# Optimization experiments

Measured on AMD Instinct MI355X. Metric: run time of the kernel, lower is better.

## Reference

```python
import jax, jax.numpy as jnp
import numpy as np

N, E = 50000, 800000
F_IN, HID, NCLS = 128, 128, 64
EPS = 1e-6


def setup_inputs() -> dict:
    key = jax.random.key(0)
    ks = jax.random.split(key, 6)
    x = jax.random.normal(ks[0], (N, F_IN), dtype=jnp.float32)
    edge_index = jax.random.randint(ks[1], (2, E), 0, N, dtype=jnp.int32)
    # GCNConv glorot init
    W1 = jax.random.normal(ks[2], (F_IN, HID), dtype=jnp.float32) * np.sqrt(2.0 / (F_IN + HID))
    b1 = jnp.zeros((HID,), jnp.float32)
    gamma1 = jnp.ones((HID,), jnp.float32)
    beta1 = jnp.zeros((HID,), jnp.float32)
    W2 = jax.random.normal(ks[3], (HID, NCLS), dtype=jnp.float32) * np.sqrt(2.0 / (HID + NCLS))
    b2 = jnp.zeros((NCLS,), jnp.float32)
    return {"x": x, "edge_index": edge_index, "W1": W1, "b1": b1,
            "gamma1": gamma1, "beta1": beta1, "W2": W2, "b2": b2}


def _gcn_conv(x, src, dst, norm, W, b, n):
    # x' = A_hat @ (x W) + b, A_hat = D^-1/2 (A+I) D^-1/2
    h = x @ W                                   # [N, out]
    msg = h[src] * norm[:, None]                # [E+N, out] gather
    out = jax.ops.segment_sum(msg, dst, num_segments=n)  # scatter-add
    return out + b


def _layer_norm(h, gamma, beta):
    mu = jnp.mean(h, axis=-1, keepdims=True)
    var = jnp.mean(jnp.square(h - mu), axis=-1, keepdims=True)
    return (h - mu) * jax.lax.rsqrt(var + EPS) * gamma + beta


def reference(x, edge_index, W1, b1, gamma1, beta1, W2, b2):
    n = x.shape[0]
    loop = jnp.arange(n, dtype=edge_index.dtype)
    src = jnp.concatenate([edge_index[0], loop])  # add self loops
    dst = jnp.concatenate([edge_index[1], loop])
    deg = jax.ops.segment_sum(jnp.ones_like(dst, jnp.float32), dst, num_segments=n)
    dinv = jnp.where(deg > 0, jax.lax.rsqrt(deg), 0.0)
    norm = dinv[src] * dinv[dst]                 # [E+N]
    h = _gcn_conv(x, src, dst, norm, W1, b1, n)
    h = jax.nn.relu(_layer_norm(h, gamma1, beta1))
    out = _gcn_conv(h, src, dst, norm, W2, b2, n)
    return out
```

## Files before the change

### kernel.cpp

```cpp
#include <hip/hip_runtime.h>


typedef float f32x2 __attribute__((ext_vector_type(2)));
typedef float f32x4 __attribute__((ext_vector_type(4)));
typedef unsigned u32x4 __attribute__((ext_vector_type(4)));
typedef __bf16 bf16x8 __attribute__((ext_vector_type(8)));

__device__ __forceinline__ unsigned short f2bf(float f) {
    unsigned u = __float_as_uint(f);
    u += 0x7FFF + ((u >> 16) & 1);
    return (unsigned short)(u >> 16);
}
__device__ __forceinline__ float bfLo(unsigned g) { return __uint_as_float(g << 16); }
__device__ __forceinline__ float bfHi(unsigned g) { return __uint_as_float(g & 0xFFFF0000u); }

__global__ __launch_bounds__(256) void cvt_wi(const float* __restrict__ W1,
                                              const float* __restrict__ W2,
                                              unsigned short* __restrict__ W1t,
                                              unsigned short* __restrict__ W2t,
                                              int* __restrict__ cnt, int n) {
    int id = blockIdx.x * 256 + threadIdx.x;
    if (id < 128 * 128) {
        int c = id >> 7, k = id & 127;
        W1t[id] = f2bf(W1[k * 128 + c]);
    } else if (id < 128 * 128 + 64 * 128) {
        int j = id - 128 * 128;
        int c = j >> 7, k = j & 127;
        W2t[j] = f2bf(W2[k * 64 + c]);
    }
    if (id < n) cnt[id] = 0;
}

__global__ void count_k(const int* __restrict__ dst, int* __restrict__ cnt,
                        int* __restrict__ rank, int e) {
    int i = blockIdx.x * blockDim.x + threadIdx.x;
    if (i < e) {
        int r = atomicAdd(&cnt[dst[i]], 1);
        __builtin_nontemporal_store(r, &rank[i]);
    }
}

__global__ __launch_bounds__(1024) void scan1_k(const int* __restrict__ cnt,
                                                int* __restrict__ incl,
                                                int* __restrict__ bsum, int n) {
    __shared__ int lds[1024];
    int t = threadIdx.x;
    int i = blockIdx.x * 1024 + t;
    int v = (i < n) ? ((cnt[i] + 15) & ~15) : 0;
    lds[t] = v;
    __syncthreads();
#pragma unroll
    for (int d = 1; d < 1024; d <<= 1) {
        int u = (t >= d) ? lds[t - d] : 0;
        __syncthreads();
        lds[t] += u;
        __syncthreads();
    }
    if (i < n) incl[i] = lds[t];
    if (t == 1023) bsum[blockIdx.x] = lds[1023];
}

__global__ __launch_bounds__(1024) void scan3_k(const int* __restrict__ cnt,
                                                const int* __restrict__ incl,
                                                const int* __restrict__ bsum,
                                                int* __restrict__ offs,
                                                float* __restrict__ dinv,
                                                unsigned* __restrict__ epk,
                                                int nb, int n) {
    __shared__ int sP;
    int t = threadIdx.x, bid = blockIdx.x;
    if (t < 64) {
        int raw = (t < nb) ? bsum[t] : 0;
        int v = raw;
#pragma unroll
        for (int d = 1; d < 64; d <<= 1) {
            int u = __shfl_up(v, d);
            if (t >= d) v += u;
        }
        if (t == bid) sP = v - raw;
    }
    __syncthreads();
    int i = bid * 1024 + t;
    if (i >= n) return;
    int c = cnt[i];
    int c16 = (c + 15) & ~15;
    int inc = sP + incl[i];
    int ex = inc - c16;
    offs[i] = ex;
    dinv[i] = rsqrtf((float)(c + 1));
    for (int j = c; j < c16; ++j)
        __builtin_nontemporal_store(0u, &epk[ex + j]);
    if (i == n - 1) offs[n] = inc;
}

__device__ __forceinline__ void dev_fill(const int* __restrict__ src,
                                         const int* __restrict__ dst,
                                         const int* __restrict__ rank,
                                         const int* __restrict__ offs,
                                         const float* __restrict__ dinv,
                                         unsigned* __restrict__ epk, int e, int bid) {
    int i = bid * 256 + threadIdx.x;
    if (i >= e) return;
    int s = src[i], d = dst[i];
    float w = dinv[s] * dinv[d];
    epk[offs[d] + rank[i]] = ((unsigned)s << 16) | (unsigned)f2bf(w);
}

template<int NT, bool CVT>
__device__ __forceinline__ void dev_gemm(const void* __restrict__ Asrc,
                                         const uint4* __restrict__ Wt,
                                         unsigned short* __restrict__ tab,
                                         int n, int bid, uint4* As) {
    int t = threadIdx.x;
    int r0 = bid * 64;
    int rows = min(64, n - r0);
#pragma unroll
    for (int it = 0; it < 4; ++it) {
        int u = it * 256 + t;
        int row = u >> 4, s = u & 15;
        uint4 v = make_uint4(0u, 0u, 0u, 0u);
        if (row < rows) {
            if constexpr (CVT) {
                const float4* X4 = (const float4*)Asrc;
                float4 a = X4[(size_t)(r0 + row) * 32 + 2 * s];
                float4 b = X4[(size_t)(r0 + row) * 32 + 2 * s + 1];
                v.x = (unsigned)f2bf(a.x) | ((unsigned)f2bf(a.y) << 16);
                v.y = (unsigned)f2bf(a.z) | ((unsigned)f2bf(a.w) << 16);
                v.z = (unsigned)f2bf(b.x) | ((unsigned)f2bf(b.y) << 16);
                v.w = (unsigned)f2bf(b.z) | ((unsigned)f2bf(b.w) << 16);
            } else {
                v = ((const uint4*)Asrc)[(size_t)(r0 + row) * 16 + s];
            }
        }
        As[row * 16 + (s ^ (row & 7))] = v;
    }
    __syncthreads();

    int wv = t >> 6, lane = t & 63;
    int arow = lane & 15;
    int kg = lane >> 4;
    int lrow = wv * 16 + arow;

    f32x4 acc[NT];
    f32x4 z = {0.f, 0.f, 0.f, 0.f};
#pragma unroll
    for (int j = 0; j < NT; ++j) acc[j] = z;

#pragma unroll
    for (int ks = 0; ks < 4; ++ks) {
        bf16x8 a = __builtin_bit_cast(bf16x8,
                       As[lrow * 16 + ((ks * 4 + kg) ^ (arow & 7))]);
#pragma unroll
        for (int tl = 0; tl < NT; ++tl) {
            bf16x8 b = __builtin_bit_cast(bf16x8,
                           Wt[(size_t)(tl * 16 + arow) * 16 + ks * 4 + kg]);
            acc[tl] = __builtin_amdgcn_mfma_f32_16x16x32_bf16(a, b, acc[tl], 0, 0, 0);
        }
    }

    int grow0 = r0 + wv * 16 + 4 * kg;
#pragma unroll
    for (int r = 0; r < 4; ++r) {
        int grow = grow0 + r;
        if (grow < n) {
            unsigned short* rowp = tab + (size_t)grow * (NT * 16) + arow;
#pragma unroll
            for (int tl = 0; tl < NT; ++tl)
                rowp[tl * 16] = f2bf(acc[tl][r]);
        }
    }
}

__global__ __launch_bounds__(256) void fill_gemm1_k(const float* __restrict__ x,
                                                    const uint4* __restrict__ W1t,
                                                    unsigned short* __restrict__ h0b,
                                                    int n, int gb,
                                                    const int* __restrict__ src,
                                                    const int* __restrict__ dst,
                                                    const int* __restrict__ rank,
                                                    const int* __restrict__ offs,
                                                    const float* __restrict__ dinv,
                                                    unsigned* __restrict__ epk, int e) {
    __shared__ uint4 As[64 * 16];
    int bid = blockIdx.x;
    if (bid < gb)
        dev_gemm<8, true>(x, W1t, h0b, n, bid, As);
    else
        dev_fill(src, dst, rank, offs, dinv, epk, e, bid - gb);
}

__global__ __launch_bounds__(256) void gemm2_k(const unsigned* __restrict__ h1b,
                                               const uint4* __restrict__ W2t,
                                               unsigned short* __restrict__ tab,
                                               int n) {
    __shared__ uint4 As[64 * 16];
    dev_gemm<4, false>(h1b, W2t, tab, n, blockIdx.x, As);
}

__global__ __launch_bounds__(256) void prop_ln(const unsigned* __restrict__ h0b,
                                               const int* __restrict__ offs,
                                               const unsigned* __restrict__ epk,
                                               const float* __restrict__ dinv,
                                               const float* __restrict__ b1,
                                               const float* __restrict__ gamma,
                                               const float* __restrict__ beta,
                                               unsigned* __restrict__ h1b, int n) {
    int wid = __builtin_amdgcn_readfirstlane((blockIdx.x * blockDim.x + threadIdx.x) >> 6);
    int lane = threadIdx.x & 63;
    if (wid >= n) return;
    float di = dinv[wid];
    unsigned self = h0b[(size_t)wid * 64 + lane];
    float a0 = bfLo(self) * di * di;
    float a1 = bfHi(self) * di * di;

    int s0 = offs[wid], s1 = offs[wid + 1];
    if (s0 < s1) {
        const u32x4* ep4 = (const u32x4*)(epk + s0);
        int nb16 = (s1 - s0) >> 4;
        u32x4 d0 = __builtin_nontemporal_load(ep4);
        u32x4 d1 = __builtin_nontemporal_load(ep4 + 1);
        u32x4 d2 = __builtin_nontemporal_load(ep4 + 2);
        u32x4 d3 = __builtin_nontemporal_load(ep4 + 3);
        for (int b = 0; b < nb16; ++b) {
            unsigned g0  = h0b[(size_t)(d0.x >> 16) * 64 + lane];
            unsigned g1  = h0b[(size_t)(d0.y >> 16) * 64 + lane];
            unsigned g2  = h0b[(size_t)(d0.z >> 16) * 64 + lane];
            unsigned g3  = h0b[(size_t)(d0.w >> 16) * 64 + lane];
            unsigned g4  = h0b[(size_t)(d1.x >> 16) * 64 + lane];
            unsigned g5  = h0b[(size_t)(d1.y >> 16) * 64 + lane];
            unsigned g6  = h0b[(size_t)(d1.z >> 16) * 64 + lane];
            unsigned g7  = h0b[(size_t)(d1.w >> 16) * 64 + lane];
            unsigned g8  = h0b[(size_t)(d2.x >> 16) * 64 + lane];
            unsigned g9  = h0b[(size_t)(d2.y >> 16) * 64 + lane];
            unsigned g10 = h0b[(size_t)(d2.z >> 16) * 64 + lane];
            unsigned g11 = h0b[(size_t)(d2.w >> 16) * 64 + lane];
            unsigned g12 = h0b[(size_t)(d3.x >> 16) * 64 + lane];
            unsigned g13 = h0b[(size_t)(d3.y >> 16) * 64 + lane];
            unsigned g14 = h0b[(size_t)(d3.z >> 16) * 64 + lane];
            unsigned g15 = h0b[(size_t)(d3.w >> 16) * 64 + lane];
            float w0  = bfLo(d0.x), w1  = bfLo(d0.y), w2  = bfLo(d0.z), w3  = bfLo(d0.w);
            float w4  = bfLo(d1.x), w5  = bfLo(d1.y), w6  = bfLo(d1.z), w7  = bfLo(d1.w);
            float w8  = bfLo(d2.x), w9  = bfLo(d2.y), w10 = bfLo(d2.z), w11 = bfLo(d2.w);
            float w12 = bfLo(d3.x), w13 = bfLo(d3.y), w14 = bfLo(d3.z), w15 = bfLo(d3.w);
            int bn = (b + 1 < nb16) ? b + 1 : 0;
            d0 = __builtin_nontemporal_load(ep4 + 4 * bn);
            d1 = __builtin_nontemporal_load(ep4 + 4 * bn + 1);
            d2 = __builtin_nontemporal_load(ep4 + 4 * bn + 2);
            d3 = __builtin_nontemporal_load(ep4 + 4 * bn + 3);
            a0 = fmaf(bfLo(g0),  w0,  a0); a1 = fmaf(bfHi(g0),  w0,  a1);
            a0 = fmaf(bfLo(g1),  w1,  a0); a1 = fmaf(bfHi(g1),  w1,  a1);
            a0 = fmaf(bfLo(g2),  w2,  a0); a1 = fmaf(bfHi(g2),  w2,  a1);
            a0 = fmaf(bfLo(g3),  w3,  a0); a1 = fmaf(bfHi(g3),  w3,  a1);
            a0 = fmaf(bfLo(g4),  w4,  a0); a1 = fmaf(bfHi(g4),  w4,  a1);
            a0 = fmaf(bfLo(g5),  w5,  a0); a1 = fmaf(bfHi(g5),  w5,  a1);
            a0 = fmaf(bfLo(g6),  w6,  a0); a1 = fmaf(bfHi(g6),  w6,  a1);
            a0 = fmaf(bfLo(g7),  w7,  a0); a1 = fmaf(bfHi(g7),  w7,  a1);
            a0 = fmaf(bfLo(g8),  w8,  a0); a1 = fmaf(bfHi(g8),  w8,  a1);
            a0 = fmaf(bfLo(g9),  w9,  a0); a1 = fmaf(bfHi(g9),  w9,  a1);
            a0 = fmaf(bfLo(g10), w10, a0); a1 = fmaf(bfHi(g10), w10, a1);
            a0 = fmaf(bfLo(g11), w11, a0); a1 = fmaf(bfHi(g11), w11, a1);
            a0 = fmaf(bfLo(g12), w12, a0); a1 = fmaf(bfHi(g12), w12, a1);
            a0 = fmaf(bfLo(g13), w13, a0); a1 = fmaf(bfHi(g13), w13, a1);
            a0 = fmaf(bfLo(g14), w14, a0); a1 = fmaf(bfHi(g14), w14, a1);
            a0 = fmaf(bfLo(g15), w15, a0); a1 = fmaf(bfHi(g15), w15, a1);
        }
    }

    a0 += b1[2 * lane];
    a1 += b1[2 * lane + 1];
    float sum = a0 + a1, sq = a0 * a0 + a1 * a1;
#pragma unroll
    for (int off = 32; off > 0; off >>= 1) {
        sum += __shfl_xor(sum, off);
        sq  += __shfl_xor(sq, off);
    }
    float mu  = sum * (1.f / 128.f);
    float var = fmaxf(sq * (1.f / 128.f) - mu * mu, 0.f);
    float rstd = rsqrtf(var + 1e-6f);
    float y0 = fmaxf((a0 - mu) * rstd * gamma[2 * lane] + beta[2 * lane], 0.f);
    float y1 = fmaxf((a1 - mu) * rstd * gamma[2 * lane + 1] + beta[2 * lane + 1], 0.f);
    unsigned pk = (unsigned)f2bf(y0) | ((unsigned)f2bf(y1) << 16);
    __builtin_nontemporal_store(pk, &h1b[(size_t)wid * 64 + lane]);
}

__global__ __launch_bounds__(256) void prop_out(const unsigned* __restrict__ h2b,
                                                const int* __restrict__ offs,
                                                const unsigned* __restrict__ epk,
                                                const float* __restrict__ dinv,
                                                const float* __restrict__ b2,
                                                float* __restrict__ out, int n) {
    int wid = __builtin_amdgcn_readfirstlane((blockIdx.x * blockDim.x + threadIdx.x) >> 6);
    int lane = threadIdx.x & 63;
    if (wid >= n) return;
    int es = lane >> 5, u = lane & 31;
    float di = dinv[wid];
    float a0 = 0.f, a1 = 0.f;
    if (es == 0) {
        unsigned self = h2b[(size_t)wid * 32 + u];
        a0 = bfLo(self) * di * di;
        a1 = bfHi(self) * di * di;
    }

    int s0 = offs[wid], s1 = offs[wid + 1];
    if (s0 < s1) {
        const u32x4* ep4 = (const u32x4*)(epk + s0);
        int nb16 = (s1 - s0) >> 4;
        u32x4 d0 = __builtin_nontemporal_load(ep4);
        u32x4 d1 = __builtin_nontemporal_load(ep4 + 1);
        u32x4 d2 = __builtin_nontemporal_load(ep4 + 2);
        u32x4 d3 = __builtin_nontemporal_load(ep4 + 3);
        for (int b = 0; b < nb16; ++b) {
            unsigned dd0 = es ? d0.y : d0.x;
            unsigned dd1 = es ? d0.w : d0.z;
            unsigned dd2 = es ? d1.y : d1.x;
            unsigned dd3 = es ? d1.w : d1.z;
            unsigned dd4 = es ? d2.y : d2.x;
            unsigned dd5 = es ? d2.w : d2.z;
            unsigned dd6 = es ? d3.y : d3.x;
            unsigned dd7 = es ? d3.w : d3.z;
            unsigned g0 = h2b[(size_t)(dd0 >> 16) * 32 + u];
            unsigned g1 = h2b[(size_t)(dd1 >> 16) * 32 + u];
            unsigned g2 = h2b[(size_t)(dd2 >> 16) * 32 + u];
            unsigned g3 = h2b[(size_t)(dd3 >> 16) * 32 + u];
            unsigned g4 = h2b[(size_t)(dd4 >> 16) * 32 + u];
            unsigned g5 = h2b[(size_t)(dd5 >> 16) * 32 + u];
            unsigned g6 = h2b[(size_t)(dd6 >> 16) * 32 + u];
            unsigned g7 = h2b[(size_t)(dd7 >> 16) * 32 + u];
            float w0 = bfLo(dd0), w1 = bfLo(dd1), w2 = bfLo(dd2), w3 = bfLo(dd3);
            float w4 = bfLo(dd4), w5 = bfLo(dd5), w6 = bfLo(dd6), w7 = bfLo(dd7);
            int bn = (b + 1 < nb16) ? b + 1 : 0;
            d0 = __builtin_nontemporal_load(ep4 + 4 * bn);
            d1 = __builtin_nontemporal_load(ep4 + 4 * bn + 1);
            d2 = __builtin_nontemporal_load(ep4 + 4 * bn + 2);
            d3 = __builtin_nontemporal_load(ep4 + 4 * bn + 3);
            a0 = fmaf(bfLo(g0), w0, a0); a1 = fmaf(bfHi(g0), w0, a1);
            a0 = fmaf(bfLo(g1), w1, a0); a1 = fmaf(bfHi(g1), w1, a1);
            a0 = fmaf(bfLo(g2), w2, a0); a1 = fmaf(bfHi(g2), w2, a1);
            a0 = fmaf(bfLo(g3), w3, a0); a1 = fmaf(bfHi(g3), w3, a1);
            a0 = fmaf(bfLo(g4), w4, a0); a1 = fmaf(bfHi(g4), w4, a1);
            a0 = fmaf(bfLo(g5), w5, a0); a1 = fmaf(bfHi(g5), w5, a1);
            a0 = fmaf(bfLo(g6), w6, a0); a1 = fmaf(bfHi(g6), w6, a1);
            a0 = fmaf(bfLo(g7), w7, a0); a1 = fmaf(bfHi(g7), w7, a1);
        }
    }

    a0 += __shfl_xor(a0, 32);
    a1 += __shfl_xor(a1, 32);
    if (es == 0) {
        f32x2 o; o.x = a0 + b2[2 * u]; o.y = a1 + b2[2 * u + 1];
        __builtin_nontemporal_store(o, &((f32x2*)out)[(size_t)wid * 32 + u]);
    }
}

extern "C" void kernel_launch(void* const* d_in, const int* in_sizes, int n_in,
                              void* d_out, int out_size, void* d_ws, size_t ws_size,
                              hipStream_t stream) {
    const float* x     = (const float*)d_in[0];
    const int*   ei    = (const int*)d_in[1];
    const float* W1    = (const float*)d_in[2];
    const float* b1    = (const float*)d_in[3];
    const float* gam   = (const float*)d_in[4];
    const float* bet   = (const float*)d_in[5];
    const float* W2    = (const float*)d_in[6];
    const float* b2    = (const float*)d_in[7];
    float* out = (float*)d_out;

    int n = in_sizes[0] / 128;
    int e = in_sizes[1] / 2;
    const int* src = ei;
    const int* dst = ei + e;
    size_t ecap = (size_t)e + 16 * (size_t)n;

    char* p = (char*)d_ws;
    auto alloc = [&](size_t bytes) {
        void* q = (void*)p;
        p += (bytes + 255) & ~(size_t)255;
        return q;
    };
    int*            cnt  = (int*)alloc((size_t)n * 4);
    int*            offs = (int*)alloc((size_t)(n + 1) * 4);
    int*            rank = (int*)alloc((size_t)e * 4);
    float*          dinv = (float*)alloc((size_t)n * 4);
    int*            incl = (int*)alloc((size_t)n * 4);
    int*            bsum = (int*)alloc(64 * 4);
    unsigned*       epk  = (unsigned*)alloc(ecap * 4);
    unsigned*       h0b  = (unsigned*)alloc((size_t)n * 64 * 4);
    unsigned*       h1b  = (unsigned*)alloc((size_t)n * 64 * 4);
    unsigned short* W1t  = (unsigned short*)alloc(128 * 128 * 2);
    unsigned short* W2t  = (unsigned short*)alloc(64 * 128 * 2);

    unsigned* h2b = h0b;

    int nb = (n + 1023) / 1024;
    int gb = (n + 63) / 64;
    int fb = (e + 255) / 256;

    cvt_wi<<<(n + 255) / 256, 256, 0, stream>>>(W1, W2, W1t, W2t, cnt, n);
    count_k<<<(e + 255) / 256, 256, 0, stream>>>(dst, cnt, rank, e);
    scan1_k<<<nb, 1024, 0, stream>>>(cnt, incl, bsum, n);
    scan3_k<<<nb, 1024, 0, stream>>>(cnt, incl, bsum, offs, dinv, epk, nb, n);
    fill_gemm1_k<<<gb + fb, 256, 0, stream>>>(x, (const uint4*)W1t,
                                              (unsigned short*)h0b, n, gb,
                                              src, dst, rank, offs, dinv, epk, e);
    prop_ln<<<(n + 3) / 4, 256, 0, stream>>>(h0b, offs, epk, dinv, b1, gam, bet, h1b, n);
    gemm2_k<<<gb, 256, 0, stream>>>(h1b, (const uint4*)W2t,
                                    (unsigned short*)h2b, n);
    prop_out<<<(n + 3) / 4, 256, 0, stream>>>(h2b, offs, epk, dinv, b2, out, n);
}
```

Before: 157.0 us.

## Bucket edge fill by destination chunk, then scatter per chunk into CSR

Edge fill becomes two phases. First, each edge is appended, via an atomic cursor, to a staging bucket for its 64-node destination chunk, along with its dst and rank. Then a new kernel scatters each bucket's records into the padded CSR array, aiming to make the final writes local instead of spread across the whole array. GEMM1 blocks are interleaved 1:4 with fill blocks, and the dinv computation moves from scan3 into scan1. The cost is an extra launch, an extra staging write and read, bucket-cursor atomics, and assumptions that fit the test sizes: fixed bucket capacity, 16-bit node ids, and fill-block count tied to gb.

```diff
diff --git a/kernel.cpp b/kernel.cpp
--- a/kernel.cpp
+++ b/kernel.cpp
@@ -3,8 +3,11 @@
 
 typedef float f32x2 __attribute__((ext_vector_type(2)));
 typedef float f32x4 __attribute__((ext_vector_type(4)));
+typedef unsigned u32x2 __attribute__((ext_vector_type(2)));
 typedef unsigned u32x4 __attribute__((ext_vector_type(4)));
 typedef __bf16 bf16x8 __attribute__((ext_vector_type(8)));
+
+#define CB_CAP 2048
 
 __device__ __forceinline__ unsigned short f2bf(float f) {
     unsigned u = __float_as_uint(f);
@@ -18,7 +21,9 @@
                                               const float* __restrict__ W2,
                                               unsigned short* __restrict__ W1t,
                                               unsigned short* __restrict__ W2t,
-                                              int* __restrict__ cnt, int n) {
+                                              int* __restrict__ cnt,
+                                              int* __restrict__ ccur,
+                                              int cbn, int n) {
     int id = blockIdx.x * 256 + threadIdx.x;
     if (id < 128 * 128) {
         int c = id >> 7, k = id & 127;
@@ -29,6 +34,7 @@
         W2t[j] = f2bf(W2[k * 64 + c]);
     }
     if (id < n) cnt[id] = 0;
+    if (id < cbn) ccur[id] = 0;
 }
 
 __global__ void count_k(const int* __restrict__ dst, int* __restrict__ cnt,
@@ -42,11 +48,13 @@
 
 __global__ __launch_bounds__(1024) void scan1_k(const int* __restrict__ cnt,
                                                 int* __restrict__ incl,
-                                                int* __restrict__ bsum, int n) {
+                                                int* __restrict__ bsum,
+                                                float* __restrict__ dinv, int n) {
     __shared__ int lds[1024];
     int t = threadIdx.x;
     int i = blockIdx.x * 1024 + t;
-    int v = (i < n) ? ((cnt[i] + 15) & ~15) : 0;
+    int c = (i < n) ? cnt[i] : 0;
+    int v = (i < n) ? ((c + 15) & ~15) : 0;
     lds[t] = v;
     __syncthreads();
 #pragma unroll
@@ -56,7 +64,10 @@
         lds[t] += u;
         __syncthreads();
     }
-    if (i < n) incl[i] = lds[t];
+    if (i < n) {
+        incl[i] = lds[t];
+        dinv[i] = rsqrtf((float)(c + 1));
+    }
     if (t == 1023) bsum[blockIdx.x] = lds[1023];
 }
 
@@ -64,7 +75,6 @@
                                                 const int* __restrict__ incl,
                                                 const int* __restrict__ bsum,
                                                 int* __restrict__ offs,
-                                                float* __restrict__ dinv,
                                                 unsigned* __restrict__ epk,
                                                 int nb, int n) {
     __shared__ int sP;
@@ -87,23 +97,42 @@
     int inc = sP + incl[i];
     int ex = inc - c16;
     offs[i] = ex;
-    dinv[i] = rsqrtf((float)(c + 1));
     for (int j = c; j < c16; ++j)
         __builtin_nontemporal_store(0u, &epk[ex + j]);
     if (i == n - 1) offs[n] = inc;
 }
 
-__device__ __forceinline__ void dev_fill(const int* __restrict__ src,
-                                         const int* __restrict__ dst,
-                                         const int* __restrict__ rank,
-                                         const int* __restrict__ offs,
-                                         const float* __restrict__ dinv,
-                                         unsigned* __restrict__ epk, int e, int bid) {
+__device__ __forceinline__ void dev_fill_a(const int* __restrict__ src,
+                                           const int* __restrict__ dst,
+                                           const int* __restrict__ rank,
+                                           const float* __restrict__ dinv,
+                                           int* __restrict__ ccur,
+                                           u32x2* __restrict__ cstage,
+                                           int e, int bid) {
     int i = bid * 256 + threadIdx.x;
     if (i >= e) return;
-    int s = src[i], d = dst[i];
+    int s = src[i], d = dst[i], r = rank[i];
     float w = dinv[s] * dinv[d];
-    epk[offs[d] + rank[i]] = ((unsigned)s << 16) | (unsigned)f2bf(w);
+    int cb = d >> 6;
+    int pos = atomicAdd(&ccur[cb], 1);
+    u32x2 rec;
+    rec.x = ((unsigned)s << 16) | (unsigned)f2bf(w);
+    rec.y = ((unsigned)d << 16) | (unsigned)r;
+    cstage[(size_t)cb * CB_CAP + pos] = rec;
+}
+
+__global__ __launch_bounds__(256) void fill_b(const u32x2* __restrict__ cstage,
+                                              const int* __restrict__ ccur,
+                                              const int* __restrict__ offs,
+                                              unsigned* __restrict__ epk) {
+    int cb = blockIdx.x;
+    int cnt = ccur[cb];
+    const u32x2* base = cstage + (size_t)cb * CB_CAP;
+    for (int j = threadIdx.x; j < cnt; j += 256) {
+        u32x2 rec = base[j];
+        unsigned d = rec.y >> 16, r = rec.y & 0xFFFFu;
+        epk[offs[d] + r] = rec.x;
+    }
 }
 
 template<int NT, bool CVT>
@@ -178,15 +207,16 @@
                                                     const int* __restrict__ src,
                                                     const int* __restrict__ dst,
                                                     const int* __restrict__ rank,
-                                                    const int* __restrict__ offs,
                                                     const float* __restrict__ dinv,
-                                                    unsigned* __restrict__ epk, int e) {
+                                                    int* __restrict__ ccur,
+                                                    u32x2* __restrict__ cstage, int e) {
     __shared__ uint4 As[64 * 16];
     int bid = blockIdx.x;
-    if (bid < gb)
-        dev_gemm<8, true>(x, W1t, h0b, n, bid, As);
+    int g = bid / 5, r = bid % 5;
+    if (r == 0 && g < gb)
+        dev_gemm<8, true>(x, W1t, h0b, n, g, As);
     else
-        dev_fill(src, dst, rank, offs, dinv, epk, e, bid - gb);
+        dev_fill_a(src, dst, rank, dinv, ccur, cstage, e, g * 4 + r - 1);
 }
 
 __global__ __launch_bounds__(256) void gemm2_k(const unsigned* __restrict__ h1b,
@@ -370,6 +400,7 @@
     const int* src = ei;
     const int* dst = ei + e;
     size_t ecap = (size_t)e + 16 * (size_t)n;
+    int cbn = (n + 63) >> 6;
 
     char* p = (char*)d_ws;
     auto alloc = [&](size_t bytes) {
@@ -377,31 +408,33 @@
         p += (bytes + 255) & ~(size_t)255;
         return q;
     };
-    int*            cnt  = (int*)alloc((size_t)n * 4);
-    int*            offs = (int*)alloc((size_t)(n + 1) * 4);
-    int*            rank = (int*)alloc((size_t)e * 4);
-    float*          dinv = (float*)alloc((size_t)n * 4);
-    int*            incl = (int*)alloc((size_t)n * 4);
-    int*            bsum = (int*)alloc(64 * 4);
-    unsigned*       epk  = (unsigned*)alloc(ecap * 4);
-    unsigned*       h0b  = (unsigned*)alloc((size_t)n * 64 * 4);
-    unsigned*       h1b  = (unsigned*)alloc((size_t)n * 64 * 4);
-    unsigned short* W1t  = (unsigned short*)alloc(128 * 128 * 2);
-    unsigned short* W2t  = (unsigned short*)alloc(64 * 128 * 2);
+    int*            cnt    = (int*)alloc((size_t)n * 4);
+    int*            offs   = (int*)alloc((size_t)(n + 1) * 4);
+    int*            rank   = (int*)alloc((size_t)e * 4);
+    float*          dinv   = (float*)alloc((size_t)n * 4);
+    int*            incl   = (int*)alloc((size_t)n * 4);
+    int*            bsum   = (int*)alloc(64 * 4);
+    int*            ccur   = (int*)alloc((size_t)cbn * 4);
+    u32x2*          cstage = (u32x2*)alloc((size_t)cbn * CB_CAP * 8);
+    unsigned*       epk    = (unsigned*)alloc(ecap * 4);
+    unsigned*       h0b    = (unsigned*)alloc((size_t)n * 64 * 4);
+    unsigned*       h1b    = (unsigned*)alloc((size_t)n * 64 * 4);
+    unsigned short* W1t    = (unsigned short*)alloc(128 * 128 * 2);
+    unsigned short* W2t    = (unsigned short*)alloc(64 * 128 * 2);
 
     unsigned* h2b = h0b;
 
     int nb = (n + 1023) / 1024;
     int gb = (n + 63) / 64;
-    int fb = (e + 255) / 256;
-
-    cvt_wi<<<(n + 255) / 256, 256, 0, stream>>>(W1, W2, W1t, W2t, cnt, n);
+
+    cvt_wi<<<(n + 255) / 256, 256, 0, stream>>>(W1, W2, W1t, W2t, cnt, ccur, cbn, n);
     count_k<<<(e + 255) / 256, 256, 0, stream>>>(dst, cnt, rank, e);
-    scan1_k<<<nb, 1024, 0, stream>>>(cnt, incl, bsum, n);
-    scan3_k<<<nb, 1024, 0, stream>>>(cnt, incl, bsum, offs, dinv, epk, nb, n);
-    fill_gemm1_k<<<gb + fb, 256, 0, stream>>>(x, (const uint4*)W1t,
-                                              (unsigned short*)h0b, n, gb,
-                                              src, dst, rank, offs, dinv, epk, e);
+    scan1_k<<<nb, 1024, 0, stream>>>(cnt, incl, bsum, dinv, n);
+    scan3_k<<<nb, 1024, 0, stream>>>(cnt, incl, bsum, offs, epk, nb, n);
+    fill_gemm1_k<<<gb * 5, 256, 0, stream>>>(x, (const uint4*)W1t,
+                                             (unsigned short*)h0b, n, gb,
+                                             src, dst, rank, dinv, ccur, cstage, e);
+    fill_b<<<cbn, 256, 0, stream>>>(cstage, ccur, offs, epk);
     prop_ln<<<(n + 3) / 4, 256, 0, stream>>>(h0b, offs, epk, dinv, b1, gam, bet, h1b, n);
     gemm2_k<<<gb, 256, 0, stream>>>(h1b, (const uint4*)W2t,
                                     (unsigned short*)h2b, n);
```

Result: slower. 326.7 us (+108.0%).
